# Optimization experiments

Hardware: AMD Instinct MI355X
Metric: run time of the kernel (lower is better)

Reference implementation:

```python
import jax, jax.numpy as jnp
import numpy as np

A, G, P, C = 250000, 64, 4096, 2
LOW, HIGH = 0.3, 0.7
BETA = 1.0 / 9.0
IMG = 800.0


def _make_boxes(key, n):
    k1, k2 = jax.random.split(key)
    xy = jax.random.uniform(k1, (n, 2), minval=0.0, maxval=IMG - 130.0)
    wh = jax.random.uniform(k2, (n, 2), minval=8.0, maxval=128.0)
    return jnp.concatenate([xy, xy + wh], axis=1)


def setup_inputs():
    ks = jax.random.split(jax.random.key(0), 11)
    return {
        "anchors": _make_boxes(ks[0], A),
        "gt_boxes": _make_boxes(ks[1], G),
        "gt_score_labels": jax.random.uniform(ks[2], (G,)),
        "gt_confidence_labels": jax.random.randint(ks[3], (G,), 0, 2),
        "objectness": jax.random.normal(ks[4], (A,)),
        "pred_bbox_deltas": jax.random.normal(ks[5], (A, 4)) * 0.1,
        "class_logits": jax.random.normal(ks[6], (P, C)),
        "box_regression": jax.random.normal(ks[7], (P, C * 4)) * 0.1,
        "roi_labels": jax.random.randint(ks[8], (P,), 0, C),
        "roi_regression_targets": jax.random.normal(ks[9], (P, 4)) * 0.1,
        "roi_scores": jax.random.uniform(ks[10], (P,)),
    }


def box_iou(a, b):
    # a: [G,4], b: [A,4] -> [G,A]
    area_a = (a[:, 2] - a[:, 0]) * (a[:, 3] - a[:, 1])
    area_b = (b[:, 2] - b[:, 0]) * (b[:, 3] - b[:, 1])
    lt = jnp.maximum(a[:, None, :2], b[None, :, :2])
    rb = jnp.minimum(a[:, None, 2:], b[None, :, 2:])
    wh = jnp.clip(rb - lt, 0.0)
    inter = wh[..., 0] * wh[..., 1]
    return inter / (area_a[:, None] + area_b[None, :] - inter)


def encode_boxes(gt, anchors):
    # torchvision BoxCoder.encode with unit weights
    aw = anchors[:, 2] - anchors[:, 0]
    ah = anchors[:, 3] - anchors[:, 1]
    acx = anchors[:, 0] + 0.5 * aw
    acy = anchors[:, 1] + 0.5 * ah
    gw = gt[:, 2] - gt[:, 0]
    gh = gt[:, 3] - gt[:, 1]
    gcx = gt[:, 0] + 0.5 * gw
    gcy = gt[:, 1] + 0.5 * gh
    return jnp.stack([(gcx - acx) / aw, (gcy - acy) / ah,
                      jnp.log(gw / aw), jnp.log(gh / ah)], axis=1)


def smooth_l1(d):
    ad = jnp.abs(d)
    return jnp.where(ad < BETA, 0.5 * d * d / BETA, ad - 0.5 * BETA)


def reference(anchors, gt_boxes, gt_score_labels, gt_confidence_labels, objectness,
              pred_bbox_deltas, class_logits, box_regression, roi_labels,
              roi_regression_targets, roi_scores):
    # ---- assign_targets_to_anchors (Matcher with low-quality matches) ----
    iou = box_iou(gt_boxes, anchors)            # [G, A]
    matched_vals = iou.max(axis=0)              # [A]
    all_matches = iou.argmax(axis=0)            # [A]
    matched_idxs = jnp.where(matched_vals < LOW, -1,
                   jnp.where(matched_vals < HIGH, -2, all_matches))
    best_per_gt = iou.max(axis=1, keepdims=True)            # [G,1]
    force = (iou == best_per_gt).any(axis=0)                # [A]
    matched_idxs = jnp.where(force, all_matches, matched_idxs)
    clamped = jnp.clip(matched_idxs, 0)
    matched_gt = gt_boxes[clamped]                          # [A,4]
    labels = (matched_idxs >= 0).astype(jnp.float32)
    labels = jnp.minimum(labels, gt_score_labels[clamped])
    labels = jnp.where(matched_idxs == -1, 0.0, labels)     # BELOW_LOW_THRESHOLD
    labels = jnp.where(matched_idxs == -2, -1.0, labels)    # BETWEEN_THRESHOLDS
    labels = jnp.where((gt_confidence_labels[clamped] == 0) & (matched_idxs >= 0), -1.0, labels)
    reg_targets = encode_boxes(matched_gt, anchors)         # [A,4]

    # ---- my_rpn_compute_loss (deterministic full pos/neg selection) ----
    pos = labels >= 1.0
    neg = labels == 0.0
    n_samp = pos.astype(jnp.float32).sum() + neg.astype(jnp.float32).sum()
    sl = smooth_l1(pred_bbox_deltas - reg_targets).sum(axis=-1)
    rpn_box_loss = (sl * pos).sum() / n_samp
    sel = pos | neg
    y = jnp.where(sel, jnp.clip(labels, 0.0, 1.0), 0.0)
    x = objectness
    bce = jnp.maximum(x, 0.0) - x * y + jnp.log1p(jnp.exp(-jnp.abs(x)))
    objectness_loss = (bce * sel).sum() / n_samp

    # ---- my_roi_loss ----
    fixed_labels = jnp.stack([1.0 - roi_scores, roi_scores], axis=1)  # [P,2]
    log_probs = jax.nn.log_softmax(class_logits, axis=1)
    classification_loss = jnp.mean(-(fixed_labels * log_probs).sum(axis=1))
    br = box_regression.reshape(P, C, 4)
    idx = jnp.broadcast_to(jnp.clip(roi_labels, 0)[:, None, None], (P, 1, 4))
    br_sel = jnp.take_along_axis(br, idx, axis=1)[:, 0]               # [P,4]
    pos_roi = (roi_labels > 0).astype(jnp.float32)
    roi_box_loss = (smooth_l1(br_sel - roi_regression_targets).sum(axis=-1) * pos_roi).sum() / P

    return jnp.stack([objectness_loss, rpn_box_loss, classification_loss, roi_box_loss])
```

## Files before the change

### kernel.cpp

```cpp
#include <hip/hip_runtime.h>
#include <hip/hip_bf16.h>
#include <math.h>

#define NA 250000
#define NG 64
#define NP 4096

#define SPAN 512
#define NB ((NA + SPAN - 1) / SPAN)
#define NBP 512
#define RBLK (NP / 256)

#define OFF_TAB    0
#define OFF_MAXARG (OFF_TAB + NG * NBP)
#define OFF_FORCE  (OFF_MAXARG + 2 * NB * SPAN)
#define FORCE_FLOATS ((NB * SPAN) / 4)
#define OFF_ROI    (OFF_FORCE + FORCE_FLOATS)
#define OFF_SUM    (OFF_ROI + RBLK * 2)


static __device__ __forceinline__ float area_of(float4 b) {
#pragma clang fp contract(off)
    return (b.z - b.x) * (b.w - b.y);
}

static __device__ __forceinline__ float iou_one(
    float gx0, float gy0, float gx1, float gy1, float ga,
    float ax0, float ay0, float ax1, float ay1, float aa)
{
#pragma clang fp contract(off)
    float ltx = fmaxf(gx0, ax0);
    float lty = fmaxf(gy0, ay0);
    float rbx = fminf(gx1, ax1);
    float rby = fminf(gy1, ay1);
    float w = fmaxf(rbx - ltx, 0.0f);
    float h = fmaxf(rby - lty, 0.0f);
    float inter = w * h;
    float uni = ga + aa - inter;
    return inter * __builtin_amdgcn_rcpf(uni);
}

static __device__ __forceinline__ float smooth_l1_f(float d) {
    const float BETA = 1.0f / 9.0f;
    float ad = fabsf(d);
    return (ad < BETA) ? (0.5f * d * d / BETA) : (ad - 0.5f * BETA);
}


__global__ __launch_bounds__(256) void kA(const float4* __restrict__ anchors,
                                          const float4* __restrict__ gt,
                                          const float* __restrict__ logits,
                                          const float* __restrict__ breg,
                                          const int* __restrict__ rlab,
                                          const float4* __restrict__ rtgt,
                                          const float* __restrict__ rsc,
                                          float* __restrict__ ws) {
    int t = threadIdx.x;
    int b = blockIdx.x;

    if (b >= NB) {
        int r = b - NB;
        if (t < NBP - NB) {
#pragma unroll
            for (int row = 0; row < 4; row++)
                ws[OFF_TAB + (4 * r + row) * NBP + NB + t] = 0.0f;
        }
        __shared__ float rbuf[4][2];
        int p = r * 256 + t;
        float l0 = logits[2 * p], l1 = logits[2 * p + 1];
        float mx = fmaxf(l0, l1);
        float lse = mx + __logf(__expf(l0 - mx) + __expf(l1 - mx));
        float s = rsc[p];
        float clsl = -((1.0f - s) * (l0 - lse) + s * (l1 - lse));

        int lbl = rlab[p];
        int cl = lbl < 0 ? 0 : lbl;
        float4 bb = *(const float4*)(breg + 8 * p + 4 * cl);
        float4 tg = rtgt[p];
        float sl = smooth_l1_f(bb.x - tg.x) + smooth_l1_f(bb.y - tg.y) +
                   smooth_l1_f(bb.z - tg.z) + smooth_l1_f(bb.w - tg.w);
        float boxl = (lbl > 0) ? sl : 0.0f;

        int lane = t & 63, w = t >> 6;
        for (int off = 32; off > 0; off >>= 1) {
            clsl += __shfl_down(clsl, off);
            boxl += __shfl_down(boxl, off);
        }
        if (lane == 0) { rbuf[w][0] = clsl; rbuf[w][1] = boxl; }
        __syncthreads();
        if (t == 0) {
            float s0 = 0.f, s1 = 0.f;
            for (int i = 0; i < 4; i++) { s0 += rbuf[i][0]; s1 += rbuf[i][1]; }
            ws[OFF_ROI + 2 * r] = s0;
            ws[OFF_ROI + 2 * r + 1] = s1;
        }
        return;
    }

    unsigned* fz = (unsigned*)(ws + OFF_FORCE);
    if (t < 128) fz[b * 128 + t] = 0u;

    int a0 = b * SPAN + t;
    int a1 = a0 + 256;
    bool ok0 = a0 < NA, ok1 = a1 < NA;
    float4 av0 = ok0 ? anchors[a0] : make_float4(0.f, 0.f, 0.f, 0.f);
    float4 av1 = ok1 ? anchors[a1] : make_float4(0.f, 0.f, 0.f, 0.f);
    float aa0 = area_of(av0);
    float aa1 = area_of(av1);

    float m[NG];
#pragma unroll
    for (int g = 0; g < NG; g++) m[g] = 0.0f;

    float max0 = -1.0f, max1 = -1.0f;
    int arg0 = 0, arg1 = 0;
#pragma unroll
    for (int g = 0; g < NG; g++) {
        float4 G = gt[g];
        float ga = area_of(G);
        float u0 = iou_one(G.x, G.y, G.z, G.w, ga, av0.x, av0.y, av0.z, av0.w, aa0);
        float u1 = iou_one(G.x, G.y, G.z, G.w, ga, av1.x, av1.y, av1.z, av1.w, aa1);
        if (u0 > max0) { max0 = u0; arg0 = g; }
        if (u1 > max1) { max1 = u1; arg1 = g; }
        m[g] = fmaxf(m[g], fmaxf(u0, u1));
    }

    float2* ma = (float2*)(ws + OFF_MAXARG);
    if (ok0) ma[a0] = make_float2(max0, __int_as_float(arg0));
    if (ok1) ma[a1] = make_float2(max1, __int_as_float(arg1));

    __shared__ float sred[4][NG];
    int lane = t & 63, w = t >> 6;
#pragma unroll
    for (int g = 0; g < NG; g++) {
        float mm = m[g];
        for (int off = 32; off > 0; off >>= 1)
            mm = fmaxf(mm, __shfl_down(mm, off));
        if (lane == 0) sred[w][g] = mm;
    }
    __syncthreads();
    if (t < NG) {
        float mm = fmaxf(fmaxf(sred[0][t], sred[1][t]),
                         fmaxf(sred[2][t], sred[3][t]));
        ws[OFF_TAB + t * NBP + b] = mm;
    }
}


__global__ __launch_bounds__(256) void kF(const float4* __restrict__ anchors,
                                          const float4* __restrict__ gt,
                                          float* __restrict__ ws) {
    __shared__ float srow[NBP];
    __shared__ float swm[4];
    __shared__ float sbest;
    __shared__ int scnt;
    __shared__ int slist[NBP];
    int t = threadIdx.x;
    int g = blockIdx.x;
    int lane = t & 63, w = t >> 6;

    const float* row = ws + OFF_TAB + g * NBP;
    float v0 = row[t], v1 = row[t + 256];
    srow[t] = v0; srow[t + 256] = v1;
    float mm = fmaxf(v0, v1);
    for (int off = 32; off > 0; off >>= 1)
        mm = fmaxf(mm, __shfl_down(mm, off));
    if (lane == 0) swm[w] = mm;
    if (t == 0) scnt = 0;
    __syncthreads();
    if (t == 0)
        sbest = fmaxf(fmaxf(swm[0], swm[1]), fmaxf(swm[2], swm[3]));
    __syncthreads();
    float best = sbest;

    if (srow[t] == best)       { int i = atomicAdd(&scnt, 1); slist[i] = t; }
    if (srow[t + 256] == best) { int i = atomicAdd(&scnt, 1); slist[i] = t + 256; }
    __syncthreads();

    float4 G = gt[g];
    float ga = area_of(G);
    char* fb = (char*)(ws + OFF_FORCE);
    int cnt = scnt;
    for (int i = 0; i < cnt; i++) {
        int s = slist[i];
        int a0 = s * SPAN + t;
        int a1 = a0 + 256;
        if (a0 < NA) {
            float4 av = anchors[a0];
            float u = iou_one(G.x, G.y, G.z, G.w, ga, av.x, av.y, av.z, av.w,
                              area_of(av));
            if (u == best) fb[a0] = 1;
        }
        if (a1 < NA) {
            float4 av = anchors[a1];
            float u = iou_one(G.x, G.y, G.z, G.w, ga, av.x, av.y, av.z, av.w,
                              area_of(av));
            if (u == best) fb[a1] = 1;
        }
    }
}


__global__ __launch_bounds__(256) void kB(const float4* __restrict__ anchors,
                                          const float* __restrict__ objness,
                                          const float4* __restrict__ pdel,
                                          const float4* __restrict__ gt,
                                          const float* __restrict__ gscore,
                                          const int* __restrict__ gconf,
                                          float* __restrict__ ws) {
    __shared__ float rbuf[4][4];
    int t = threadIdx.x;
    int b = blockIdx.x;
    int lane = t & 63, w = t >> 6;
    const float2* ma = (const float2*)(ws + OFF_MAXARG);
    const char* fb = (const char*)(ws + OFF_FORCE);

    float posf = 0.f, negf = 0.f, slpos = 0.f, bces = 0.f;
#pragma unroll
    for (int k = 0; k < 2; k++) {
        int a = b * SPAN + k * 256 + t;
        if (a >= NA) continue;
        float2 mv = ma[a];
        float maxv = mv.x;
        int arg = __float_as_int(mv.y);
        bool force = fb[a] != 0;

        int matched = (maxv < 0.3f) ? -1 : ((maxv < 0.7f) ? -2 : arg);
        if (force) matched = arg;
        int cl = matched < 0 ? 0 : matched;

        float4 Ac = gt[cl];
        float score = gscore[cl];
        int conf = gconf[cl];
        float label = (matched >= 0) ? 1.0f : 0.0f;
        label = fminf(label, score);
        if (matched == -1) label = 0.0f;
        if (matched == -2) label = -1.0f;
        if (conf == 0 && matched >= 0) label = -1.0f;

        bool pos = (label >= 1.0f);
        bool neg = (label == 0.0f);
        bool sel = pos || neg;

        float4 av = anchors[a];
        float aw = av.z - av.x, ah = av.w - av.y;
        float acx = av.x + 0.5f * aw, acy = av.y + 0.5f * ah;
        float gw = Ac.z - Ac.x, gh = Ac.w - Ac.y;
        float gcx = Ac.x + 0.5f * gw, gcy = Ac.y + 0.5f * gh;
        float t0 = (gcx - acx) / aw;
        float t1 = (gcy - acy) / ah;
        float t2 = __logf(gw / aw);
        float t3 = __logf(gh / ah);

        float4 pd = pdel[a];
        float sl = smooth_l1_f(pd.x - t0) + smooth_l1_f(pd.y - t1) +
                   smooth_l1_f(pd.z - t2) + smooth_l1_f(pd.w - t3);

        float x = objness[a];
        float y = sel ? fminf(fmaxf(label, 0.0f), 1.0f) : 0.0f;
        float bce = fmaxf(x, 0.0f) - x * y + __logf(1.0f + __expf(-fabsf(x)));

        if (pos) { posf += 1.0f; slpos += sl; }
        if (neg) negf += 1.0f;
        if (sel) bces += bce;
    }

    for (int off = 32; off > 0; off >>= 1) {
        posf  += __shfl_down(posf, off);
        negf  += __shfl_down(negf, off);
        slpos += __shfl_down(slpos, off);
        bces  += __shfl_down(bces, off);
    }
    if (lane == 0) { rbuf[w][0] = posf; rbuf[w][1] = negf; rbuf[w][2] = slpos; rbuf[w][3] = bces; }
    __syncthreads();
    if (t == 0) {
        float s0 = 0.f, s1 = 0.f, s2 = 0.f, s3 = 0.f;
        for (int i = 0; i < 4; i++) { s0 += rbuf[i][0]; s1 += rbuf[i][1]; s2 += rbuf[i][2]; s3 += rbuf[i][3]; }
        float* r = ws + OFF_SUM + 4 * b;
        r[0] = s0; r[1] = s1; r[2] = s2; r[3] = s3;
    }
}


__global__ __launch_bounds__(256) void kC(const float* __restrict__ ws,
                                          float* __restrict__ out) {
    __shared__ double sred[4][6];
    int t = threadIdx.x;
    int lane = t & 63, w = t >> 6;
    double a0 = 0, a1 = 0, a2 = 0, a3 = 0, c0 = 0, c1 = 0;
    for (int r = t; r < NB; r += 256) {
        const float4 v = *(const float4*)(ws + OFF_SUM + 4 * r);
        a0 += v.x; a1 += v.y; a2 += v.z; a3 += v.w;
    }
    if (t < RBLK) {
        c0 = ws[OFF_ROI + 2 * t];
        c1 = ws[OFF_ROI + 2 * t + 1];
    }
    for (int off = 32; off > 0; off >>= 1) {
        a0 += __shfl_down(a0, off);
        a1 += __shfl_down(a1, off);
        a2 += __shfl_down(a2, off);
        a3 += __shfl_down(a3, off);
        c0 += __shfl_down(c0, off);
        c1 += __shfl_down(c1, off);
    }
    if (lane == 0) {
        sred[w][0] = a0; sred[w][1] = a1; sred[w][2] = a2;
        sred[w][3] = a3; sred[w][4] = c0; sred[w][5] = c1;
    }
    __syncthreads();
    if (t == 0) {
        double s[6] = {0, 0, 0, 0, 0, 0};
        for (int i = 0; i < 4; i++)
            for (int j = 0; j < 6; j++) s[j] += sred[i][j];
        double n = s[0] + s[1];
        out[0] = (float)(s[3] / n);
        out[1] = (float)(s[2] / n);
        out[2] = (float)(s[4] / (double)NP);
        out[3] = (float)(s[5] / (double)NP);
    }
}

extern "C" void kernel_launch(void* const* d_in, const int* in_sizes, int n_in,
                              void* d_out, int out_size, void* d_ws, size_t ws_size,
                              hipStream_t stream) {
    const float4* anchors = (const float4*)d_in[0];
    const float4* gt      = (const float4*)d_in[1];
    const float*  gscore  = (const float*)d_in[2];
    const int*    gconf   = (const int*)d_in[3];
    const float*  objness = (const float*)d_in[4];
    const float4* pdel    = (const float4*)d_in[5];
    const float*  clog    = (const float*)d_in[6];
    const float*  breg    = (const float*)d_in[7];
    const int*    rlab    = (const int*)d_in[8];
    const float4* rtgt    = (const float4*)d_in[9];
    const float*  rsc     = (const float*)d_in[10];

    float* ws = (float*)d_ws;
    float* out = (float*)d_out;

    kA<<<NB + RBLK, 256, 0, stream>>>(anchors, gt, clog, breg, rlab, rtgt, rsc, ws);
    kF<<<NG, 256, 0, stream>>>(anchors, gt, ws);
    kB<<<NB, 256, 0, stream>>>(anchors, objness, pdel, gt, gscore, gconf, ws);
    kC<<<1, 256, 0, stream>>>(ws, out);
}
```

Before: 111.2 us.

## Fold force-match detection into kB and finalize with last-block reduction

Removes the separate force-match kernel and its byte-flag buffer. Each kB block now recomputes the per-GT best IoU from the block-max table and rechecks the IoU of its own anchors only for the GT candidates whose best lies in that block. The final reduction kernel is also merged into kB through an atomic counter and a last-block pattern, so four launches become two. In exchange, every block redundantly scans the 64x512 table, and the correctness of the final sum now depends on the threadfence and atomic counter ordering.

```diff
diff --git a/kernel.cpp b/kernel.cpp
--- a/kernel.cpp
+++ b/kernel.cpp
@@ -13,10 +13,9 @@
 
 #define OFF_TAB    0
 #define OFF_MAXARG (OFF_TAB + NG * NBP)
-#define OFF_FORCE  (OFF_MAXARG + 2 * NB * SPAN)
-#define FORCE_FLOATS ((NB * SPAN) / 4)
-#define OFF_ROI    (OFF_FORCE + FORCE_FLOATS)
+#define OFF_ROI    (OFF_MAXARG + 2 * NB * SPAN)
 #define OFF_SUM    (OFF_ROI + RBLK * 2)
+#define OFF_CNT    (OFF_SUM + NB * 4)
 
 
 static __device__ __forceinline__ float area_of(float4 b) {
@@ -60,6 +59,7 @@
 
     if (b >= NB) {
         int r = b - NB;
+        if (r == 0 && t == 0) *(int*)(ws + OFF_CNT) = 0;
         if (t < NBP - NB) {
 #pragma unroll
             for (int row = 0; row < 4; row++)
@@ -96,9 +96,6 @@
         }
         return;
     }
-
-    unsigned* fz = (unsigned*)(ws + OFF_FORCE);
-    if (t < 128) fz[b * 128 + t] = 0u;
 
     int a0 = b * SPAN + t;
     int a1 = a0 + 256;
@@ -147,73 +144,51 @@
 }
 
 
-__global__ __launch_bounds__(256) void kF(const float4* __restrict__ anchors,
-                                          const float4* __restrict__ gt,
-                                          float* __restrict__ ws) {
-    __shared__ float srow[NBP];
-    __shared__ float swm[4];
-    __shared__ float sbest;
-    __shared__ int scnt;
-    __shared__ int slist[NBP];
-    int t = threadIdx.x;
-    int g = blockIdx.x;
-    int lane = t & 63, w = t >> 6;
-
-    const float* row = ws + OFF_TAB + g * NBP;
-    float v0 = row[t], v1 = row[t + 256];
-    srow[t] = v0; srow[t + 256] = v1;
-    float mm = fmaxf(v0, v1);
-    for (int off = 32; off > 0; off >>= 1)
-        mm = fmaxf(mm, __shfl_down(mm, off));
-    if (lane == 0) swm[w] = mm;
-    if (t == 0) scnt = 0;
-    __syncthreads();
-    if (t == 0)
-        sbest = fmaxf(fmaxf(swm[0], swm[1]), fmaxf(swm[2], swm[3]));
-    __syncthreads();
-    float best = sbest;
-
-    if (srow[t] == best)       { int i = atomicAdd(&scnt, 1); slist[i] = t; }
-    if (srow[t + 256] == best) { int i = atomicAdd(&scnt, 1); slist[i] = t + 256; }
-    __syncthreads();
-
-    float4 G = gt[g];
-    float ga = area_of(G);
-    char* fb = (char*)(ws + OFF_FORCE);
-    int cnt = scnt;
-    for (int i = 0; i < cnt; i++) {
-        int s = slist[i];
-        int a0 = s * SPAN + t;
-        int a1 = a0 + 256;
-        if (a0 < NA) {
-            float4 av = anchors[a0];
-            float u = iou_one(G.x, G.y, G.z, G.w, ga, av.x, av.y, av.z, av.w,
-                              area_of(av));
-            if (u == best) fb[a0] = 1;
-        }
-        if (a1 < NA) {
-            float4 av = anchors[a1];
-            float u = iou_one(G.x, G.y, G.z, G.w, ga, av.x, av.y, av.z, av.w,
-                              area_of(av));
-            if (u == best) fb[a1] = 1;
-        }
-    }
-}
-
-
 __global__ __launch_bounds__(256) void kB(const float4* __restrict__ anchors,
                                           const float* __restrict__ objness,
                                           const float4* __restrict__ pdel,
                                           const float4* __restrict__ gt,
                                           const float* __restrict__ gscore,
                                           const int* __restrict__ gconf,
-                                          float* __restrict__ ws) {
+                                          float* __restrict__ ws,
+                                          float* __restrict__ out) {
+    __shared__ float sbest[NG];
+    __shared__ int   scand[NG];
+    __shared__ int   scnt;
     __shared__ float rbuf[4][4];
+    __shared__ bool  islast;
+
     int t = threadIdx.x;
     int b = blockIdx.x;
     int lane = t & 63, w = t >> 6;
+
+    if (t == 0) scnt = 0;
+
+    {
+        int g = t >> 2, quad = t & 3;
+        const float4* rowv = (const float4*)(ws + OFF_TAB + g * NBP + quad * 128);
+        float mm = 0.0f;
+#pragma unroll
+        for (int j = 0; j < 32; j++) {
+            float4 v = rowv[j];
+            mm = fmaxf(mm, fmaxf(fmaxf(v.x, v.y), fmaxf(v.z, v.w)));
+        }
+        mm = fmaxf(mm, __shfl_xor(mm, 1));
+        mm = fmaxf(mm, __shfl_xor(mm, 2));
+        if (quad == 0) sbest[g] = mm;
+    }
+    __syncthreads();
+
+    if (t < NG) {
+        if (ws[OFF_TAB + t * NBP + b] == sbest[t]) {
+            int i = atomicAdd(&scnt, 1);
+            scand[i] = t;
+        }
+    }
+    __syncthreads();
+    int cnt = scnt;
+
     const float2* ma = (const float2*)(ws + OFF_MAXARG);
-    const char* fb = (const char*)(ws + OFF_FORCE);
 
     float posf = 0.f, negf = 0.f, slpos = 0.f, bces = 0.f;
 #pragma unroll
@@ -223,7 +198,18 @@
         float2 mv = ma[a];
         float maxv = mv.x;
         int arg = __float_as_int(mv.y);
-        bool force = fb[a] != 0;
+
+        float4 av = anchors[a];
+        float aa = area_of(av);
+
+        bool force = false;
+        for (int i = 0; i < cnt; i++) {
+            int g = scand[i];
+            float4 G = gt[g];
+            float ga = area_of(G);
+            float u = iou_one(G.x, G.y, G.z, G.w, ga, av.x, av.y, av.z, av.w, aa);
+            force |= (u == sbest[g]);
+        }
 
         int matched = (maxv < 0.3f) ? -1 : ((maxv < 0.7f) ? -2 : arg);
         if (force) matched = arg;
@@ -242,7 +228,6 @@
         bool neg = (label == 0.0f);
         bool sel = pos || neg;
 
-        float4 av = anchors[a];
         float aw = av.z - av.x, ah = av.w - av.y;
         float acx = av.x + 0.5f * aw, acy = av.y + 0.5f * ah;
         float gw = Ac.z - Ac.x, gh = Ac.w - Ac.y;
@@ -278,15 +263,15 @@
         for (int i = 0; i < 4; i++) { s0 += rbuf[i][0]; s1 += rbuf[i][1]; s2 += rbuf[i][2]; s3 += rbuf[i][3]; }
         float* r = ws + OFF_SUM + 4 * b;
         r[0] = s0; r[1] = s1; r[2] = s2; r[3] = s3;
-    }
-}
-
-
-__global__ __launch_bounds__(256) void kC(const float* __restrict__ ws,
-                                          float* __restrict__ out) {
-    __shared__ double sred[4][6];
-    int t = threadIdx.x;
-    int lane = t & 63, w = t >> 6;
+        __threadfence();
+        int prev = atomicAdd((int*)(ws + OFF_CNT), 1);
+        islast = (prev == NB - 1);
+    }
+    __syncthreads();
+    if (!islast) return;
+    __threadfence();
+
+    __shared__ double sredc[4][6];
     double a0 = 0, a1 = 0, a2 = 0, a3 = 0, c0 = 0, c1 = 0;
     for (int r = t; r < NB; r += 256) {
         const float4 v = *(const float4*)(ws + OFF_SUM + 4 * r);
@@ -305,14 +290,14 @@
         c1 += __shfl_down(c1, off);
     }
     if (lane == 0) {
-        sred[w][0] = a0; sred[w][1] = a1; sred[w][2] = a2;
-        sred[w][3] = a3; sred[w][4] = c0; sred[w][5] = c1;
+        sredc[w][0] = a0; sredc[w][1] = a1; sredc[w][2] = a2;
+        sredc[w][3] = a3; sredc[w][4] = c0; sredc[w][5] = c1;
     }
     __syncthreads();
     if (t == 0) {
         double s[6] = {0, 0, 0, 0, 0, 0};
         for (int i = 0; i < 4; i++)
-            for (int j = 0; j < 6; j++) s[j] += sred[i][j];
+            for (int j = 0; j < 6; j++) s[j] += sredc[i][j];
         double n = s[0] + s[1];
         out[0] = (float)(s[3] / n);
         out[1] = (float)(s[2] / n);
@@ -340,7 +325,5 @@
     float* out = (float*)d_out;
 
     kA<<<NB + RBLK, 256, 0, stream>>>(anchors, gt, clog, breg, rlab, rtgt, rsc, ws);
-    kF<<<NG, 256, 0, stream>>>(anchors, gt, ws);
-    kB<<<NB, 256, 0, stream>>>(anchors, objness, pdel, gt, gscore, gconf, ws);
-    kC<<<1, 256, 0, stream>>>(ws, out);
-}
+    kB<<<NB, 256, 0, stream>>>(anchors, objness, pdel, gt, gscore, gconf, ws, out);
+}
```

Measured after the change: 123.0 us. 1.11x slower.
